# Performance work log

Measured on AMD Instinct MI355X. Metric: run time of the kernel, lower is better.

## Reference

```python
import jax, jax.numpy as jnp
import numpy as np

C = 256
C8 = C // 8

def setup_inputs() -> dict:
    key = jax.random.key(0)
    ks = jax.random.split(key, 8)
    a = jax.random.normal(ks[0], (4, C, 64, 64), dtype=jnp.float32)
    s = 1.0 / np.sqrt(C)
    b_w = jax.random.normal(ks[1], (C8, C), dtype=jnp.float32) * s
    b_b = jnp.zeros((C8,), dtype=jnp.float32)
    c_w = jax.random.normal(ks[2], (C8, C), dtype=jnp.float32) * s
    c_b = jnp.zeros((C8,), dtype=jnp.float32)
    d_w = jax.random.normal(ks[3], (C, C), dtype=jnp.float32) * s
    d_b = jnp.zeros((C,), dtype=jnp.float32)
    alpha = jnp.zeros((1,), dtype=jnp.float32) + 0.5  # nonzero so attention path is exercised
    return {"a": a, "b_w": b_w, "b_b": b_b, "c_w": c_w, "c_b": c_b, "d_w": d_w, "d_b": d_b, "alpha": alpha}

def _conv1x1(x, w, b):
    # x: [n, c, h, w], w: [o, c] -> [n, o, h, w]
    return jnp.einsum('nchw,oc->nohw', x, w) + b[None, :, None, None]

def reference(a, b_w, b_b, c_w, c_b, d_w, d_b, alpha):
    n, chan, h, w = a.shape
    nhw = h * w
    b = _conv1x1(a, b_w, b_b).reshape(n, -1, nhw)   # [n, C/8, nhw]
    c = _conv1x1(a, c_w, c_b).reshape(n, -1, nhw)   # [n, C/8, nhw]
    k = jnp.einsum('nci,ncj->nij', b, c)            # [n, nhw, nhw]
    s = jax.nn.softmax(k, axis=-1)
    d = _conv1x1(a, d_w, d_b).reshape(n, -1, nhw)   # [n, C, nhw]
    kl = jnp.einsum('ncj,nij->nci', d, s)           # d @ s^T
    kl = kl.reshape(n, chan, h, w)
    return alpha * kl + a
```

## Files before the change

### kernel.cpp

```cpp
#include <hip/hip_runtime.h>
#include <hip/hip_bf16.h>

#define CCH 256
#define CQK 32
#define NHW 4096

typedef float f32x4 __attribute__((ext_vector_type(4)));
typedef _Float16 hv8 __attribute__((ext_vector_type(8)));
typedef _Float16 hv4 __attribute__((ext_vector_type(4)));
typedef __fp16 fv2 __attribute__((ext_vector_type(2)));

__device__ __forceinline__ unsigned enc_f32(float f) {
    unsigned u = __float_as_uint(f);
    return (u & 0x80000000u) ? ~u : (u | 0x80000000u);
}
__device__ __forceinline__ float dec_f32(unsigned u) {
    return __uint_as_float((u & 0x80000000u) ? (u ^ 0x80000000u) : ~u);
}

typedef __attribute__((address_space(3))) unsigned int lds_u32_t;
typedef __attribute__((address_space(1))) const unsigned int glb_u32_t;
__device__ __forceinline__ void gll16(const _Float16* gp, _Float16* lp) {
    __builtin_amdgcn_global_load_lds((glb_u32_t*)gp, (lds_u32_t*)lp, 16, 0, 0);
}

__global__ __launch_bounds__(256) void prep_kernel(
    const float* __restrict__ b_w, const float* __restrict__ c_w,
    const float* __restrict__ d_w, _Float16* __restrict__ Wh,
    unsigned* __restrict__ m_enc)
{
    const int bid = blockIdx.x, tid = threadIdx.x;
    if (bid < 80) {
        const int idx = (bid * 256 + tid) * 4;
        const int row = idx >> 8, col = idx & 255;
        const float* src = (row < 32) ? (b_w + row * CCH + col)
                         : (row < 64) ? (c_w + (row - 32) * CCH + col)
                                      : (d_w + (row - 64) * CCH + col);
        const float scl = (row < 32) ? 1.4426950408889634f : 1.0f;
        float4 v = *reinterpret_cast<const float4*>(src);
        _Float16* dst = Wh + (size_t)row * CCH + col;
        dst[0] = (_Float16)(v.x * scl); dst[1] = (_Float16)(v.y * scl);
        dst[2] = (_Float16)(v.z * scl); dst[3] = (_Float16)(v.w * scl);
    } else {
        m_enc[(bid - 80) * 256 + tid] = 0u;
    }
}

__global__ __launch_bounds__(256) void proj_kernel(
    const float* __restrict__ a, const _Float16* __restrict__ Wh,
    const float* __restrict__ b_b, const float* __restrict__ c_b,
    const float* __restrict__ d_b,
    _Float16* __restrict__ bqT, _Float16* __restrict__ ckT,
    _Float16* __restrict__ dv)
{
    __shared__ _Float16 aT[32][CCH + 24];

    const int n    = blockIdx.x >> 7;
    const int i0   = (blockIdx.x & 127) << 5;
    const int tid  = threadIdx.x;
    const int lane = tid & 63;
    const int wave = tid >> 6;
    const int l15  = lane & 15;
    const int quad = lane >> 4;

    {
        const float* ap = a + (size_t)(n*CCH + tid)*NHW + i0;
        #pragma unroll
        for (int j = 0; j < 8; ++j) {
            float4 v = *reinterpret_cast<const float4*>(ap + j*4);
            aT[j*4+0][tid] = (_Float16)v.x;
            aT[j*4+1][tid] = (_Float16)v.y;
            aT[j*4+2][tid] = (_Float16)v.z;
            aT[j*4+3][tid] = (_Float16)v.w;
        }
    }
    __syncthreads();

    const f32x4 zf = {0.f, 0.f, 0.f, 0.f};
    f32x4 acc[5][2];
    #pragma unroll
    for (int t = 0; t < 5; ++t) { acc[t][0] = zf; acc[t][1] = zf; }

    const int ch0w = wave * 80;

    #pragma unroll
    for (int ks = 0; ks < 8; ++ks) {
        const int k0 = ks * 32;
        hv8 af0 = *reinterpret_cast<const hv8*>(&aT[l15][k0 + quad*8]);
        hv8 af1 = *reinterpret_cast<const hv8*>(&aT[16 + l15][k0 + quad*8]);
        #pragma unroll
        for (int t = 0; t < 5; ++t) {
            const int ch0 = ch0w + t*16;
            hv8 bf = *reinterpret_cast<const hv8*>(
                Wh + (size_t)(ch0 + l15)*CCH + k0 + quad*8);
            acc[t][0] = __builtin_amdgcn_mfma_f32_16x16x32_f16(af0, bf, acc[t][0], 0, 0, 0);
            acc[t][1] = __builtin_amdgcn_mfma_f32_16x16x32_f16(af1, bf, acc[t][1], 0, 0, 0);
        }
    }

    const int pos_b = i0 + quad*4;
    #pragma unroll
    for (int t = 0; t < 5; ++t) {
        const int ch0 = ch0w + t*16;
        if (ch0 < 64) {
            const float* bias_arr = (ch0 < 32) ? b_b : c_b;
            _Float16*    outp     = (ch0 < 32) ? bqT : ckT;
            const int    ch       = (ch0 & 31) + l15;
            const float  bias     = bias_arr[ch] *
                ((ch0 < 32) ? 1.4426950408889634f : 1.0f);
            #pragma unroll
            for (int nf = 0; nf < 2; ++nf) {
                #pragma unroll
                for (int r = 0; r < 4; ++r) {
                    const int pos = pos_b + nf*16 + r;
                    outp[((size_t)n*NHW + pos)*CQK + ch] =
                        (_Float16)(acc[t][nf][r] + bias);
                }
            }
        } else {
            const int ch   = ch0 - 64 + l15;
            const float bias = d_b[ch];
            #pragma unroll
            for (int nf = 0; nf < 2; ++nf) {
                hv4 v = { (_Float16)(acc[t][nf][0] + bias),
                          (_Float16)(acc[t][nf][1] + bias),
                          (_Float16)(acc[t][nf][2] + bias),
                          (_Float16)(acc[t][nf][3] + bias) };
                *reinterpret_cast<hv4*>(
                    dv + ((size_t)n*CCH + ch)*NHW + pos_b + nf*16) = v;
            }
        }
    }
}

__global__ __launch_bounds__(256) void rowmax_kernel(
    const _Float16* __restrict__ bqT, const _Float16* __restrict__ ckT,
    unsigned* __restrict__ m_enc)
{
    const int bx   = blockIdx.x;
    const int n    = bx >> 8;
    const int qt   = (bx >> 2) & 63;
    const int ks   = bx & 3;
    const int q0   = qt << 6;
    const int tid  = threadIdx.x;
    const int wave = tid >> 6;
    const int lane = tid & 63;
    const int l15  = lane & 15;
    const int quad = lane >> 4;

    const f32x4 zf = {0.f, 0.f, 0.f, 0.f};
    const hv8 qf = *reinterpret_cast<const hv8*>(
        bqT + ((size_t)n*NHW + q0 + wave*16 + l15)*CQK + quad*8);

    float mx = -1e30f;

    for (int kt = ks*16; kt < ks*16 + 16; ++kt) {
        const int k0 = kt << 6;
        #pragma unroll
        for (int f = 0; f < 4; ++f) {
            hv8 kf = *reinterpret_cast<const hv8*>(
                ckT + ((size_t)n*NHW + k0 + f*16 + l15)*CQK + quad*8);
            f32x4 s = __builtin_amdgcn_mfma_f32_16x16x32_f16(kf, qf, zf, 0, 0, 0);
            mx = fmaxf(mx, fmaxf(fmaxf(s[0], s[1]), fmaxf(s[2], s[3])));
        }
    }
    mx = fmaxf(mx, __shfl_xor(mx, 16, 64));
    mx = fmaxf(mx, __shfl_xor(mx, 32, 64));
    if (lane < 16)
        atomicMax(&m_enc[n*NHW + q0 + wave*16 + l15], enc_f32(mx));
}

__global__ __launch_bounds__(512, 2) void attn_kernel(
    const _Float16* __restrict__ bqT, const _Float16* __restrict__ ckT,
    const _Float16* __restrict__ dv, const unsigned* __restrict__ m_enc,
    const float* __restrict__ a, const float* __restrict__ alpha_p,
    float* __restrict__ out)
{
    __shared__ __align__(16) char smem[141312];

    const int bx   = ((blockIdx.x & 7) << 5) | (blockIdx.x >> 3);
    const int n    = bx >> 6;
    const int cg   = (bx >> 5) & 1;
    const int qt   = bx & 31;
    const int q0b  = qt << 7;
    const int co0  = cg << 7;
    const int tid  = threadIdx.x;
    const int wave = tid >> 6;
    const int g    = wave >> 1;
    const int qw   = wave & 1;
    const int lane = tid & 63;
    const int l15  = lane & 15;
    const int quad = lane >> 4;
    const int kg0  = g << 10;

    _Float16* vbuf = (_Float16*)(smem + (g << 14));
    _Float16* pb   = (_Float16*)(smem + 65536 + wave*9216);
    float*    lbuf = (float*)(smem + 139264);

    const f32x4 zf = {0.f, 0.f, 0.f, 0.f};
    const _Float16 one_h = (_Float16)1.0f;
    const hv8 ones = { one_h, one_h, one_h, one_h, one_h, one_h, one_h, one_h };

    hv8 qf[4]; float mneg[4];
    #pragma unroll
    for (int X = 0; X < 4; ++X) {
        const int q = q0b + qw*64 + X*16 + l15;
        qf[X] = *reinterpret_cast<const hv8*>(
            bqT + ((size_t)n*NHW + q)*CQK + quad*8);
        mneg[X] = -dec_f32(m_enc[n*NHW + q]);
    }

    f32x4 acc[4][8];
    #pragma unroll
    for (int X = 0; X < 4; ++X)
        #pragma unroll
        for (int t = 0; t < 8; ++t) acc[X][t] = zf;
    f32x4 accL[4];
    #pragma unroll
    for (int X = 0; X < 4; ++X) accL[X] = zf;

    const int rl8 = lane >> 3;
    const _Float16* dvs = dv
        + (size_t)(n*CCH + co0 + qw*64 + rl8)*NHW + kg0 + 8*((lane & 7) ^ rl8);
    _Float16* ldsb = (_Float16*)(smem + (g << 14) + qw*8192);

    const _Float16* ckbase = ckT + ((size_t)(n*NHW + kg0 + l15))*CQK + quad*8;

    const int c0h = ((quad*16) ^ ((l15 & 7) << 4)) >> 1;
    const int c1h = ((64 + quad*16) ^ ((l15 & 7) << 4)) >> 1;

    auto softmax_tile = [&](const hv8* kf) {
        #pragma unroll
        for (int X = 0; X < 4; ++X) {
            const f32x4 minit = {mneg[X], mneg[X], mneg[X], mneg[X]};
            #pragma unroll
            for (int f = 0; f < 4; ++f) {
                f32x4 s = __builtin_amdgcn_mfma_f32_16x16x32_f16(
                    kf[f], qf[X], minit, 0, 0, 0);
                float p0 = __builtin_amdgcn_exp2f(s[0]);
                float p1 = __builtin_amdgcn_exp2f(s[1]);
                float p2 = __builtin_amdgcn_exp2f(s[2]);
                float p3 = __builtin_amdgcn_exp2f(s[3]);
                fv2 lo = __builtin_amdgcn_cvt_pkrtz(p0, p1);
                fv2 hi = __builtin_amdgcn_cvt_pkrtz(p2, p3);
                uint2 w;
                w.x = __builtin_bit_cast(unsigned, lo);
                w.y = __builtin_bit_cast(unsigned, hi);
                *reinterpret_cast<uint2*>(
                    pb + X*1152 + l15*72 + f*16 + quad*4) = w;
            }
        }
    };

    hv8 pf0[4], pf1[4];
    auto read_pf = [&]() {
        #pragma unroll
        for (int X = 0; X < 4; ++X) {
            pf0[X] = *reinterpret_cast<const hv8*>(pb + X*1152 + l15*72 + quad*8);
            pf1[X] = *reinterpret_cast<const hv8*>(pb + X*1152 + l15*72 + 32 + quad*8);
        }
    };

    auto stage = [&](int kt) {
        #pragma unroll
        for (int j = 0; j < 8; ++j)
            gll16(dvs + (size_t)(j*8)*NHW + kt*64, ldsb + (size_t)(j*8)*64);
    };

    auto load_kf = [&](int key0, hv8* kf) {
        #pragma unroll
        for (int f = 0; f < 4; ++f)
            kf[f] = *reinterpret_cast<const hv8*>(
                ckbase + (size_t)(key0 + f*16)*CQK);
    };

    {
        stage(0);
        hv8 kf0[4];
        load_kf(0, kf0);
        softmax_tile(kf0);
        read_pf();
    }
    __syncthreads();

    for (int kt = 0; kt < 16; ++kt) {
        hv8 kfn[4];
        if (kt < 15) load_kf((kt + 1)*64, kfn);

        #pragma unroll
        for (int t = 0; t < 8; ++t) {
            const _Float16* vr = vbuf + (t*16 + l15)*64;
            hv8 d0 = *reinterpret_cast<const hv8*>(vr + c0h);
            #pragma unroll
            for (int X = 0; X < 4; ++X)
                acc[X][t] = __builtin_amdgcn_mfma_f32_16x16x32_f16(
                    pf0[X], d0, acc[X][t], 0, 0, 0);
            hv8 d1 = *reinterpret_cast<const hv8*>(vr + c1h);
            #pragma unroll
            for (int X = 0; X < 4; ++X)
                acc[X][t] = __builtin_amdgcn_mfma_f32_16x16x32_f16(
                    pf1[X], d1, acc[X][t], 0, 0, 0);
        }
        #pragma unroll
        for (int X = 0; X < 4; ++X) {
            accL[X] = __builtin_amdgcn_mfma_f32_16x16x32_f16(pf0[X], ones, accL[X], 0, 0, 0);
            accL[X] = __builtin_amdgcn_mfma_f32_16x16x32_f16(pf1[X], ones, accL[X], 0, 0, 0);
        }

        if (kt < 15) {
            softmax_tile(kfn);
            __syncthreads();
            stage(kt + 1);
            read_pf();
            __syncthreads();
        }
    }

    __syncthreads();
    float* buf1 = (float*)smem;
    float* buf2 = (float*)(smem + 67584);

    if (l15 == 0) {
        #pragma unroll
        for (int X = 0; X < 4; ++X)
            *reinterpret_cast<float4*>(&lbuf[g*128 + qw*64 + X*16 + quad*4]) =
                *reinterpret_cast<float4*>(&accL[X]);
    }
    if (g == 1 || g == 3) {
        float* b = (g == 1) ? buf1 : buf2;
        #pragma unroll
        for (int X = 0; X < 4; ++X)
            #pragma unroll
            for (int t = 0; t < 8; ++t)
                *reinterpret_cast<float4*>(
                    &b[(t*16 + l15)*132 + qw*64 + X*16 + quad*4]) =
                    *reinterpret_cast<float4*>(&acc[X][t]);
    }
    __syncthreads();
    if (g == 0 || g == 2) {
        float* b = (g == 0) ? buf1 : buf2;
        #pragma unroll
        for (int X = 0; X < 4; ++X)
            #pragma unroll
            for (int t = 0; t < 8; ++t) {
                float4 p = *reinterpret_cast<float4*>(
                    &b[(t*16 + l15)*132 + qw*64 + X*16 + quad*4]);
                acc[X][t][0] += p.x; acc[X][t][1] += p.y;
                acc[X][t][2] += p.z; acc[X][t][3] += p.w;
            }
    }
    __syncthreads();
    if (g == 2) {
        #pragma unroll
        for (int X = 0; X < 4; ++X)
            #pragma unroll
            for (int t = 0; t < 8; ++t)
                *reinterpret_cast<float4*>(
                    &buf1[(t*16 + l15)*132 + qw*64 + X*16 + quad*4]) =
                    *reinterpret_cast<float4*>(&acc[X][t]);
    }
    __syncthreads();
    if (g == 0) {
        const float alpha = alpha_p[0];
        #pragma unroll
        for (int X = 0; X < 4; ++X) {
            const int qloc = qw*64 + X*16 + quad*4;
            #pragma unroll
            for (int t = 0; t < 8; ++t) {
                float4 p = *reinterpret_cast<float4*>(
                    &buf1[(t*16 + l15)*132 + qloc]);
                acc[X][t][0] += p.x; acc[X][t][1] += p.y;
                acc[X][t][2] += p.z; acc[X][t][3] += p.w;
            }
            float4 l0 = *reinterpret_cast<float4*>(&lbuf[0*128 + qloc]);
            float4 l1 = *reinterpret_cast<float4*>(&lbuf[1*128 + qloc]);
            float4 l2 = *reinterpret_cast<float4*>(&lbuf[2*128 + qloc]);
            float4 l3 = *reinterpret_cast<float4*>(&lbuf[3*128 + qloc]);
            f32x4 rl;
            rl[0] = alpha / (l0.x + l1.x + l2.x + l3.x);
            rl[1] = alpha / (l0.y + l1.y + l2.y + l3.y);
            rl[2] = alpha / (l0.z + l1.z + l2.z + l3.z);
            rl[3] = alpha / (l0.w + l1.w + l2.w + l3.w);
            #pragma unroll
            for (int t = 0; t < 8; ++t) {
                const size_t off =
                    ((size_t)(n*CCH + co0 + t*16 + l15))*NHW + q0b + qloc;
                float4 av = *reinterpret_cast<const float4*>(a + off);
                float4 o;
                o.x = acc[X][t][0]*rl[0] + av.x;
                o.y = acc[X][t][1]*rl[1] + av.y;
                o.z = acc[X][t][2]*rl[2] + av.z;
                o.w = acc[X][t][3]*rl[3] + av.w;
                *reinterpret_cast<float4*>(out + off) = o;
            }
        }
    }
}

extern "C" void kernel_launch(void* const* d_in, const int* in_sizes, int n_in,
                              void* d_out, int out_size, void* d_ws, size_t ws_size,
                              hipStream_t stream)
{
    const float* a    = (const float*)d_in[0];
    const float* b_w  = (const float*)d_in[1];
    const float* b_b  = (const float*)d_in[2];
    const float* c_w  = (const float*)d_in[3];
    const float* c_b  = (const float*)d_in[4];
    const float* d_w  = (const float*)d_in[5];
    const float* d_b  = (const float*)d_in[6];
    const float* alp  = (const float*)d_in[7];
    float* out = (float*)d_out;

    _Float16* bqT  = (_Float16*)d_ws;
    _Float16* ckT  = bqT + (size_t)4*NHW*CQK;
    _Float16* dv   = ckT + (size_t)4*NHW*CQK;
    unsigned* m_enc = (unsigned*)(dv + (size_t)4*CCH*NHW);
    _Float16* Wh   = (_Float16*)(m_enc + 4*NHW);

    prep_kernel<<<144, 256, 0, stream>>>(b_w, c_w, d_w, Wh, m_enc);
    proj_kernel<<<512, 256, 0, stream>>>(a, Wh, b_b, c_b, d_b, bqT, ckT, dv);
    rowmax_kernel<<<1024, 256, 0, stream>>>(bqT, ckT, m_enc);
    attn_kernel<<<256, 512, 0, stream>>>(bqT, ckT, dv, m_enc, a, alp, out);
}
```

Baseline: 175.7 us.

## Fuse row-max pass into attention kernel, dropping separate rowmax kernel and atomics

Removes the standalone rowmax kernel and the m_enc buffer. Each attention block now computes the per-query max over its key range, then combines the four key-group partials through shared memory before the softmax pass. This saves a kernel launch, the global atomics and the zero-init. In exchange the QK^T max work is recomputed by both channel-group blocks and runs with lower parallelism inside the attention kernel.

```diff
diff --git a/kernel.cpp b/kernel.cpp
--- a/kernel.cpp
+++ b/kernel.cpp
@@ -9,14 +9,6 @@
 typedef _Float16 hv8 __attribute__((ext_vector_type(8)));
 typedef _Float16 hv4 __attribute__((ext_vector_type(4)));
 typedef __fp16 fv2 __attribute__((ext_vector_type(2)));
-
-__device__ __forceinline__ unsigned enc_f32(float f) {
-    unsigned u = __float_as_uint(f);
-    return (u & 0x80000000u) ? ~u : (u | 0x80000000u);
-}
-__device__ __forceinline__ float dec_f32(unsigned u) {
-    return __uint_as_float((u & 0x80000000u) ? (u ^ 0x80000000u) : ~u);
-}
 
 typedef __attribute__((address_space(3))) unsigned int lds_u32_t;
 typedef __attribute__((address_space(1))) const unsigned int glb_u32_t;
@@ -26,24 +18,19 @@
 
 __global__ __launch_bounds__(256) void prep_kernel(
     const float* __restrict__ b_w, const float* __restrict__ c_w,
-    const float* __restrict__ d_w, _Float16* __restrict__ Wh,
-    unsigned* __restrict__ m_enc)
+    const float* __restrict__ d_w, _Float16* __restrict__ Wh)
 {
     const int bid = blockIdx.x, tid = threadIdx.x;
-    if (bid < 80) {
-        const int idx = (bid * 256 + tid) * 4;
-        const int row = idx >> 8, col = idx & 255;
-        const float* src = (row < 32) ? (b_w + row * CCH + col)
-                         : (row < 64) ? (c_w + (row - 32) * CCH + col)
-                                      : (d_w + (row - 64) * CCH + col);
-        const float scl = (row < 32) ? 1.4426950408889634f : 1.0f;
-        float4 v = *reinterpret_cast<const float4*>(src);
-        _Float16* dst = Wh + (size_t)row * CCH + col;
-        dst[0] = (_Float16)(v.x * scl); dst[1] = (_Float16)(v.y * scl);
-        dst[2] = (_Float16)(v.z * scl); dst[3] = (_Float16)(v.w * scl);
-    } else {
-        m_enc[(bid - 80) * 256 + tid] = 0u;
-    }
+    const int idx = (bid * 256 + tid) * 4;
+    const int row = idx >> 8, col = idx & 255;
+    const float* src = (row < 32) ? (b_w + row * CCH + col)
+                     : (row < 64) ? (c_w + (row - 32) * CCH + col)
+                                  : (d_w + (row - 64) * CCH + col);
+    const float scl = (row < 32) ? 1.4426950408889634f : 1.0f;
+    float4 v = *reinterpret_cast<const float4*>(src);
+    _Float16* dst = Wh + (size_t)row * CCH + col;
+    dst[0] = (_Float16)(v.x * scl); dst[1] = (_Float16)(v.y * scl);
+    dst[2] = (_Float16)(v.z * scl); dst[3] = (_Float16)(v.w * scl);
 }
 
 __global__ __launch_bounds__(256) void proj_kernel(
@@ -133,46 +120,9 @@
     }
 }
 
-__global__ __launch_bounds__(256) void rowmax_kernel(
-    const _Float16* __restrict__ bqT, const _Float16* __restrict__ ckT,
-    unsigned* __restrict__ m_enc)
-{
-    const int bx   = blockIdx.x;
-    const int n    = bx >> 8;
-    const int qt   = (bx >> 2) & 63;
-    const int ks   = bx & 3;
-    const int q0   = qt << 6;
-    const int tid  = threadIdx.x;
-    const int wave = tid >> 6;
-    const int lane = tid & 63;
-    const int l15  = lane & 15;
-    const int quad = lane >> 4;
-
-    const f32x4 zf = {0.f, 0.f, 0.f, 0.f};
-    const hv8 qf = *reinterpret_cast<const hv8*>(
-        bqT + ((size_t)n*NHW + q0 + wave*16 + l15)*CQK + quad*8);
-
-    float mx = -1e30f;
-
-    for (int kt = ks*16; kt < ks*16 + 16; ++kt) {
-        const int k0 = kt << 6;
-        #pragma unroll
-        for (int f = 0; f < 4; ++f) {
-            hv8 kf = *reinterpret_cast<const hv8*>(
-                ckT + ((size_t)n*NHW + k0 + f*16 + l15)*CQK + quad*8);
-            f32x4 s = __builtin_amdgcn_mfma_f32_16x16x32_f16(kf, qf, zf, 0, 0, 0);
-            mx = fmaxf(mx, fmaxf(fmaxf(s[0], s[1]), fmaxf(s[2], s[3])));
-        }
-    }
-    mx = fmaxf(mx, __shfl_xor(mx, 16, 64));
-    mx = fmaxf(mx, __shfl_xor(mx, 32, 64));
-    if (lane < 16)
-        atomicMax(&m_enc[n*NHW + q0 + wave*16 + l15], enc_f32(mx));
-}
-
 __global__ __launch_bounds__(512, 2) void attn_kernel(
     const _Float16* __restrict__ bqT, const _Float16* __restrict__ ckT,
-    const _Float16* __restrict__ dv, const unsigned* __restrict__ m_enc,
+    const _Float16* __restrict__ dv,
     const float* __restrict__ a, const float* __restrict__ alpha_p,
     float* __restrict__ out)
 {
@@ -201,13 +151,57 @@
     const _Float16 one_h = (_Float16)1.0f;
     const hv8 ones = { one_h, one_h, one_h, one_h, one_h, one_h, one_h, one_h };
 
-    hv8 qf[4]; float mneg[4];
+    hv8 qf[4];
     #pragma unroll
     for (int X = 0; X < 4; ++X) {
         const int q = q0b + qw*64 + X*16 + l15;
         qf[X] = *reinterpret_cast<const hv8*>(
             bqT + ((size_t)n*NHW + q)*CQK + quad*8);
-        mneg[X] = -dec_f32(m_enc[n*NHW + q]);
+    }
+
+    const _Float16* ckbase = ckT + ((size_t)(n*NHW + kg0 + l15))*CQK + quad*8;
+
+    float mneg[4];
+    {
+        float mx[4];
+        #pragma unroll
+        for (int X = 0; X < 4; ++X) mx[X] = -1e30f;
+        for (int kt = 0; kt < 16; ++kt) {
+            #pragma unroll
+            for (int f = 0; f < 4; ++f) {
+                hv8 kf = *reinterpret_cast<const hv8*>(
+                    ckbase + (size_t)(kt*64 + f*16)*CQK);
+                #pragma unroll
+                for (int X = 0; X < 4; ++X) {
+                    f32x4 s = __builtin_amdgcn_mfma_f32_16x16x32_f16(
+                        kf, qf[X], zf, 0, 0, 0);
+                    mx[X] = fmaxf(mx[X],
+                        fmaxf(fmaxf(s[0], s[1]), fmaxf(s[2], s[3])));
+                }
+            }
+        }
+        #pragma unroll
+        for (int X = 0; X < 4; ++X) {
+            mx[X] = fmaxf(mx[X], __shfl_xor(mx[X], 16, 64));
+            mx[X] = fmaxf(mx[X], __shfl_xor(mx[X], 32, 64));
+        }
+        if (lane < 16) {
+            #pragma unroll
+            for (int X = 0; X < 4; ++X)
+                lbuf[(g*2 + qw)*64 + X*16 + l15] = mx[X];
+        }
+        __syncthreads();
+        #pragma unroll
+        for (int X = 0; X < 4; ++X) {
+            const int qi = qw*64 + X*16 + l15;
+            float m0 = lbuf[(0*2 + qw)*64 + X*16 + l15];
+            float m1 = lbuf[(1*2 + qw)*64 + X*16 + l15];
+            float m2 = lbuf[(2*2 + qw)*64 + X*16 + l15];
+            float m3 = lbuf[(3*2 + qw)*64 + X*16 + l15];
+            (void)qi;
+            mneg[X] = -fmaxf(fmaxf(m0, m1), fmaxf(m2, m3));
+        }
+        __syncthreads();
     }
 
     f32x4 acc[4][8];
@@ -223,8 +217,6 @@
     const _Float16* dvs = dv
         + (size_t)(n*CCH + co0 + qw*64 + rl8)*NHW + kg0 + 8*((lane & 7) ^ rl8);
     _Float16* ldsb = (_Float16*)(smem + (g << 14) + qw*8192);
-
-    const _Float16* ckbase = ckT + ((size_t)(n*NHW + kg0 + l15))*CQK + quad*8;
 
     const int c0h = ((quad*16) ^ ((l15 & 7) << 4)) >> 1;
     const int c1h = ((64 + quad*16) ^ ((l15 & 7) << 4)) >> 1;
@@ -414,11 +406,9 @@
     _Float16* bqT  = (_Float16*)d_ws;
     _Float16* ckT  = bqT + (size_t)4*NHW*CQK;
     _Float16* dv   = ckT + (size_t)4*NHW*CQK;
-    unsigned* m_enc = (unsigned*)(dv + (size_t)4*CCH*NHW);
-    _Float16* Wh   = (_Float16*)(m_enc + 4*NHW);
-
-    prep_kernel<<<144, 256, 0, stream>>>(b_w, c_w, d_w, Wh, m_enc);
+    _Float16* Wh   = dv + (size_t)4*CCH*NHW;
+
+    prep_kernel<<<80, 256, 0, stream>>>(b_w, c_w, d_w, Wh);
     proj_kernel<<<512, 256, 0, stream>>>(a, Wh, b_b, c_b, d_b, bqT, ckT, dv);
-    rowmax_kernel<<<1024, 256, 0, stream>>>(bqT, ckT, m_enc);
-    attn_kernel<<<256, 512, 0, stream>>>(bqT, ckT, dv, m_enc, a, alp, out);
+    attn_kernel<<<256, 512, 0, stream>>>(bqT, ckT, dv, a, alp, out);
 }
```

Measured after the change: 165.5 us. 5.8% less time.
